# Kernel optimization log

Hardware: AMD Instinct MI355X
Metric: run time of the kernel (lower is better)

The kernel has to match this reference:

```python
import jax, jax.numpy as jnp
import numpy as np

N_NODES = 100000
N_EDGES = 1600000
IN_DIM = 256
OUT_DIM = 64
NEG_SLOPE = 0.01  # torch F.leaky_relu default


def setup_inputs() -> dict:
    key = jax.random.key(0)
    k1, k2, k3, k4, k5 = jax.random.split(key, 5)
    h = jax.random.normal(k1, (N_NODES, IN_DIM), dtype=jnp.float32)
    # Kaiming-ish small init for linear weights
    W = jax.random.normal(k2, (OUT_DIM, IN_DIM), dtype=jnp.float32) / np.sqrt(IN_DIM)
    A = jax.random.normal(k3, (1, 2 * OUT_DIM), dtype=jnp.float32) / np.sqrt(2 * OUT_DIM)
    src = jax.random.randint(k4, (N_EDGES,), 0, N_NODES, dtype=jnp.int32)
    dst = jax.random.randint(k5, (N_EDGES,), 0, N_NODES, dtype=jnp.int32)
    return {"h": h, "W": W, "A": A, "src": src, "dst": dst}


def reference(h, W, A, src, dst):
    n = h.shape[0]
    # fc (no bias): z = h @ W^T -> [N, out]
    z = h @ W.T
    # attn_fc on cat(z_src, z_dst): split A into src/dst halves to avoid concat
    a_src, a_dst = A[0, :OUT_DIM], A[0, OUT_DIM:]
    s_node = z @ a_src  # [N]
    d_node = z @ a_dst  # [N]
    e = s_node[src] + d_node[dst]  # [E] raw attention logits per edge
    e = jnp.where(e >= 0, e, NEG_SLOPE * e)  # leaky_relu
    # segment softmax over incoming edges of each dst node (numerically stable)
    e_max = jax.ops.segment_max(e, dst, num_segments=n)  # -inf for empty segments
    e_max = jnp.where(jnp.isfinite(e_max), e_max, 0.0)
    e_exp = jnp.exp(e - e_max[dst])
    denom = jax.ops.segment_sum(e_exp, dst, num_segments=n)
    alpha = e_exp / jnp.where(denom > 0, denom, 1.0)[dst]  # [E]
    # weighted scatter-sum of source features; nodes with no in-edges get 0
    out = jax.ops.segment_sum(alpha[:, None] * z[src], dst, num_segments=n)
    return out
```

## Files before the change

### kernel.cpp

```cpp
#include <hip/hip_runtime.h>

#define N_IN 256
#define N_OUT 64
#define NEG_SLOPE 0.01f
#define BSHIFT 9
#define BSIZE 512
#define MAXBUCK 256

typedef __attribute__((ext_vector_type(8))) short short8v;
typedef __attribute__((ext_vector_type(4))) float float4v;

__device__ inline short f32_to_bf16_rtne(float f) {
    unsigned u = __float_as_uint(f);
    unsigned r = (u + 0x7FFFu + ((u >> 16) & 1u)) >> 16;
    return (short)r;
}
__device__ inline float bf16_to_f32(short s) {
    return __uint_as_float(((unsigned)(unsigned short)s) << 16);
}

constexpr int GM = 64;
constexpr int KP = 264;

__global__ __launch_bounds__(256) void gemm_zsd_mfma(
    const float* __restrict__ h, const float* __restrict__ W,
    const float* __restrict__ A,
    unsigned short* __restrict__ zb, float* __restrict__ s_node, float* __restrict__ d_node,
    int n_nodes)
{
    __shared__ short hA[GM * KP];
    __shared__ short wB[N_OUT * KP];
    const int t = threadIdx.x;
    const int row0 = blockIdx.x * GM;

    for (int j = 0; j < 8; ++j) {
        const int f  = j * 256 + t;
        const int r  = f >> 5;
        const int c8 = f & 31;

        int grow = row0 + r;
        if (grow >= n_nodes) grow = n_nodes - 1;
        const float4* ph = reinterpret_cast<const float4*>(h + (size_t)grow * N_IN + c8 * 8);
        float4 h0 = ph[0], h1 = ph[1];
        short8v pkh;
        pkh[0] = f32_to_bf16_rtne(h0.x); pkh[1] = f32_to_bf16_rtne(h0.y);
        pkh[2] = f32_to_bf16_rtne(h0.z); pkh[3] = f32_to_bf16_rtne(h0.w);
        pkh[4] = f32_to_bf16_rtne(h1.x); pkh[5] = f32_to_bf16_rtne(h1.y);
        pkh[6] = f32_to_bf16_rtne(h1.z); pkh[7] = f32_to_bf16_rtne(h1.w);
        *reinterpret_cast<short8v*>(&hA[r * KP + c8 * 8]) = pkh;

        const float4* pw = reinterpret_cast<const float4*>(W + (size_t)r * N_IN + c8 * 8);
        float4 w0 = pw[0], w1 = pw[1];
        short8v pkw;
        pkw[0] = f32_to_bf16_rtne(w0.x); pkw[1] = f32_to_bf16_rtne(w0.y);
        pkw[2] = f32_to_bf16_rtne(w0.z); pkw[3] = f32_to_bf16_rtne(w0.w);
        pkw[4] = f32_to_bf16_rtne(w1.x); pkw[5] = f32_to_bf16_rtne(w1.y);
        pkw[6] = f32_to_bf16_rtne(w1.z); pkw[7] = f32_to_bf16_rtne(w1.w);
        *reinterpret_cast<short8v*>(&wB[r * KP + c8 * 8]) = pkw;
    }
    __syncthreads();

    const int w  = t >> 6;
    const int l  = t & 63;
    const int lr = l & 15;
    const int lk = l >> 4;

    float4v acc[4] = {{0.f,0.f,0.f,0.f},{0.f,0.f,0.f,0.f},
                      {0.f,0.f,0.f,0.f},{0.f,0.f,0.f,0.f}};

    for (int kk = 0; kk < 8; ++kk) {
        const int kbase = kk * 32 + lk * 8;
        const short8v a = *reinterpret_cast<const short8v*>(&hA[(w * 16 + lr) * KP + kbase]);
#pragma unroll
        for (int n = 0; n < 4; ++n) {
            const short8v b = *reinterpret_cast<const short8v*>(&wB[(n * 16 + lr) * KP + kbase]);
            acc[n] = __builtin_amdgcn_mfma_f32_16x16x32_bf16(a, b, acc[n], 0, 0, 0);
        }
    }

    float as[4], ad[4];
#pragma unroll
    for (int n = 0; n < 4; ++n) {
        as[n] = A[n * 16 + lr];
        ad[n] = A[N_OUT + n * 16 + lr];
    }

    float sv[4] = {0.f,0.f,0.f,0.f}, dv[4] = {0.f,0.f,0.f,0.f};
#pragma unroll
    for (int n = 0; n < 4; ++n) {
#pragma unroll
        for (int r = 0; r < 4; ++r) {
            const float v = acc[n][r];
            const int grow = row0 + w * 16 + lk * 4 + r;
            if (grow < n_nodes)
                zb[(size_t)grow * N_OUT + n * 16 + lr] = (unsigned short)f32_to_bf16_rtne(v);
            sv[r] = fmaf(v, as[n], sv[r]);
            dv[r] = fmaf(v, ad[n], dv[r]);
        }
    }
#pragma unroll
    for (int off = 1; off < 16; off <<= 1) {
#pragma unroll
        for (int r = 0; r < 4; ++r) {
            sv[r] += __shfl_xor(sv[r], off);
            dv[r] += __shfl_xor(dv[r], off);
        }
    }
    if (lr == 0) {
#pragma unroll
        for (int r = 0; r < 4; ++r) {
            const int grow = row0 + w * 16 + lk * 4 + r;
            if (grow < n_nodes) { s_node[grow] = sv[r]; d_node[grow] = dv[r]; }
        }
    }
}

__global__ __launch_bounds__(256) void hist_bucket(
    const int* __restrict__ dst, int* __restrict__ bcount, int n_edges)
{
    __shared__ int cnt[MAXBUCK];
    const int t = threadIdx.x;
    for (int i = t; i < MAXBUCK; i += 256) cnt[i] = 0;
    __syncthreads();
    int i = blockIdx.x * 256 + t;
    const int stride = gridDim.x * 256;
    for (; i < n_edges; i += stride)
        atomicAdd(&cnt[dst[i] >> BSHIFT], 1);
    __syncthreads();
    for (int j = t; j < MAXBUCK; j += 256)
        if (cnt[j]) atomicAdd(&bcount[j], cnt[j]);
}

__global__ __launch_bounds__(256) void scan_buckets(
    const int* __restrict__ bcount, int* __restrict__ bbase,
    int* __restrict__ bcursor, int nbuck, int n_edges)
{
    __shared__ int tmp[256];
    const int t = threadIdx.x;
    const int v = (t < nbuck) ? bcount[t] : 0;
    tmp[t] = v;
    __syncthreads();
    for (int off = 1; off < 256; off <<= 1) {
        int x = (t >= off) ? tmp[t - off] : 0;
        __syncthreads();
        tmp[t] += x;
        __syncthreads();
    }
    if (t < nbuck) {
        const int excl = tmp[t] - v;
        bbase[t] = excl;
        bcursor[t] = excl;
    }
    if (t == 0) bbase[nbuck] = n_edges;
}

__global__ __launch_bounds__(256) void bucket_scatter(
    const int* __restrict__ src, const int* __restrict__ dst,
    const float* __restrict__ s_node, const float* __restrict__ d_node,
    int* __restrict__ bcursor, int2* __restrict__ ebuf, int n_edges, int nbuck)
{
    __shared__ int cnt[MAXBUCK];
    __shared__ int wcur[MAXBUCK];
    const int t = threadIdx.x;
    const int chunk = (n_edges + gridDim.x - 1) / gridDim.x;
    const int lo = blockIdx.x * chunk;
    const int hi = min(lo + chunk, n_edges);

    for (int i = t; i < MAXBUCK; i += 256) cnt[i] = 0;
    __syncthreads();
    for (int i = lo + t; i < hi; i += 256)
        atomicAdd(&cnt[dst[i] >> BSHIFT], 1);
    __syncthreads();
    for (int i = t; i < nbuck; i += 256)
        wcur[i] = cnt[i] ? atomicAdd(&bcursor[i], cnt[i]) : 0;
    __syncthreads();
    for (int i = lo + t; i < hi; i += 256) {
        const int d = dst[i];
        const int s = src[i];
        float e = s_node[s] + d_node[d];
        e = (e >= 0.f) ? e : NEG_SLOPE * e;
        const float pe = __expf(e);
        const int b = d >> BSHIFT;
        const int pos = atomicAdd(&wcur[b], 1);
        ebuf[pos] = make_int2(((d & (BSIZE - 1)) << 23) | s, __float_as_int(pe));
    }
}

__global__ __launch_bounds__(1024) void bucket_bin(
    const int2* __restrict__ ebuf, const int* __restrict__ bbase,
    int2* __restrict__ ebuf2, int* __restrict__ segend, int n_nodes)
{
    __shared__ int dcnt[BSIZE];
    __shared__ int dscan[BSIZE];
    __shared__ int dcur[BSIZE];
    const int t = threadIdx.x;
    const int b = blockIdx.x;
    const int lo = bbase[b];
    const int hi = bbase[b + 1];

    if (t < BSIZE) dcnt[t] = 0;
    __syncthreads();
    for (int i = lo + t; i < hi; i += 1024)
        atomicAdd(&dcnt[((unsigned)ebuf[i].x) >> 23], 1);
    __syncthreads();
    const int v = (t < BSIZE) ? dcnt[t] : 0;
    if (t < BSIZE) dscan[t] = v;
    __syncthreads();
    for (int off = 1; off < BSIZE; off <<= 1) {
        int x = (t >= off && t < BSIZE) ? dscan[t - off] : 0;
        __syncthreads();
        if (t < BSIZE) dscan[t] += x;
        __syncthreads();
    }
    if (t < BSIZE) {
        const int d = b * BSIZE + t;
        if (d < n_nodes) segend[d] = lo + dscan[t];
        dcur[t] = lo + dscan[t] - v;
    }
    __syncthreads();
    for (int i = lo + t; i < hi; i += 1024) {
        const int2 e = ebuf[i];
        const unsigned x = (unsigned)e.x;
        const int pos = atomicAdd(&dcur[x >> 23], 1);
        ebuf2[pos] = make_int2((int)(x & 0x7FFFFFu), e.y);
    }
}

__global__ __launch_bounds__(256) void gather_accum(
    const int2* __restrict__ edges, const int* __restrict__ segend,
    const unsigned short* __restrict__ zb, float* __restrict__ out, int n_nodes)
{
    const int wave = (blockIdx.x * 256 + threadIdx.x) >> 6;
    const int lane = threadIdx.x & 63;
    if (wave >= n_nodes) return;
    const int sub = lane >> 3;
    const int l8  = lane & 7;
    const int end   = segend[wave];
    const int start = (wave == 0) ? 0 : segend[wave - 1];

    float acc[8] = {0.f,0.f,0.f,0.f,0.f,0.f,0.f,0.f};
    float denom = 0.f;
    int i = start + sub;
    for (; i + 8 < end; i += 16) {
        const int2 e0 = edges[i];
        const int2 e1 = edges[i + 8];
        const short8v z0 = *reinterpret_cast<const short8v*>(zb + (size_t)e0.x * N_OUT + l8 * 8);
        const short8v z1 = *reinterpret_cast<const short8v*>(zb + (size_t)e1.x * N_OUT + l8 * 8);
        const float p0 = __int_as_float(e0.y);
        const float p1 = __int_as_float(e1.y);
        denom += p0 + p1;
#pragma unroll
        for (int j = 0; j < 8; ++j) {
            acc[j] = fmaf(p0, bf16_to_f32(z0[j]), acc[j]);
            acc[j] = fmaf(p1, bf16_to_f32(z1[j]), acc[j]);
        }
    }
    for (; i < end; i += 8) {
        const int2 e0 = edges[i];
        const short8v z0 = *reinterpret_cast<const short8v*>(zb + (size_t)e0.x * N_OUT + l8 * 8);
        const float p0 = __int_as_float(e0.y);
        denom += p0;
#pragma unroll
        for (int j = 0; j < 8; ++j)
            acc[j] = fmaf(p0, bf16_to_f32(z0[j]), acc[j]);
    }
#pragma unroll
    for (int off = 8; off < 64; off <<= 1) {
#pragma unroll
        for (int j = 0; j < 8; ++j)
            acc[j] += __shfl_xor(acc[j], off);
        denom += __shfl_xor(denom, off);
    }
    if (sub == 0) {
        const float inv = (end > start) ? 1.f / denom : 0.f;
        float4 r0, r1;
        r0.x = acc[0] * inv; r0.y = acc[1] * inv; r0.z = acc[2] * inv; r0.w = acc[3] * inv;
        r1.x = acc[4] * inv; r1.y = acc[5] * inv; r1.z = acc[6] * inv; r1.w = acc[7] * inv;
        float4* po = reinterpret_cast<float4*>(out + (size_t)wave * N_OUT + l8 * 8);
        po[0] = r0; po[1] = r1;
    }
}

extern "C" void kernel_launch(void* const* d_in, const int* in_sizes, int n_in,
                              void* d_out, int out_size, void* d_ws, size_t ws_size,
                              hipStream_t stream) {
    const float* h = (const float*)d_in[0];
    const float* W = (const float*)d_in[1];
    const float* A = (const float*)d_in[2];
    const int* src = (const int*)d_in[3];
    const int* dst = (const int*)d_in[4];
    float* out = (float*)d_out;

    const int n_nodes = in_sizes[0] / N_IN;
    const int n_edges = in_sizes[3];
    const int nbuck = (n_nodes + BSIZE - 1) / BSIZE;

    char* ws = (char*)d_ws;
    unsigned short* zb = (unsigned short*)ws;  ws += (size_t)n_nodes * N_OUT * 2;
    float* s_node  = (float*)ws;  ws += (size_t)n_nodes * 4;
    float* d_node  = (float*)ws;  ws += (size_t)n_nodes * 4;
    int*   segend  = (int*)ws;    ws += (size_t)n_nodes * 4;
    int*   bcount  = (int*)ws;    ws += MAXBUCK * 4;
    int*   bbase   = (int*)ws;    ws += (MAXBUCK + 2) * 4;
    int*   bcursor = (int*)ws;    ws += MAXBUCK * 4;
    ws = (char*)(((uintptr_t)ws + 15) & ~(uintptr_t)15);
    int2*  ebuf    = (int2*)ws;   ws += (size_t)n_edges * 8;
    int2*  ebuf2   = (int2*)ws;

    hipMemsetAsync(bcount, 0, MAXBUCK * sizeof(int), stream);

    gemm_zsd_mfma<<<(n_nodes + GM - 1) / GM, 256, 0, stream>>>(h, W, A, zb, s_node, d_node, n_nodes);

    hist_bucket<<<256, 256, 0, stream>>>(dst, bcount, n_edges);

    scan_buckets<<<1, 256, 0, stream>>>(bcount, bbase, bcursor, nbuck, n_edges);

    bucket_scatter<<<256, 256, 0, stream>>>(src, dst, s_node, d_node, bcursor, ebuf, n_edges, nbuck);

    bucket_bin<<<nbuck, 1024, 0, stream>>>(ebuf, bbase, ebuf2, segend, n_nodes);

    gather_accum<<<(n_nodes * 64 + 255) / 256, 256, 0, stream>>>(ebuf2, segend, zb, out, n_nodes);
}
```

Before: 285.4 us.

## Fuse per-bucket binning with gather-accumulate, staging sorted edges in LDS

Merges the bucket_bin and gather_accum kernels into one bucket_gather kernel. Each block bins its bucket's edges by destination into shared memory, falling back to global memory when the bucket exceeds CAP, and then its 16 waves loop over the bucket's destination nodes to accumulate. Bucket size is halved to 256 nodes so a bucket's edges (about 4096 on average) fit in LDS, and the scan kernel is widened to handle up to 512 buckets. This removes the global write and re-read of the sorted edge list, the segend array, and one kernel launch. In exchange it runs far fewer, larger blocks for the gather phase, with imbalance between waves and heavy LDS use that may limit occupancy.

```diff
diff --git a/kernel.cpp b/kernel.cpp
--- a/kernel.cpp
+++ b/kernel.cpp
@@ -3,9 +3,10 @@
 #define N_IN 256
 #define N_OUT 64
 #define NEG_SLOPE 0.01f
-#define BSHIFT 9
-#define BSIZE 512
-#define MAXBUCK 256
+#define BSHIFT 8
+#define BSIZE 256
+#define MAXBUCK 512
+#define CAP 5120
 
 typedef __attribute__((ext_vector_type(8))) short short8v;
 typedef __attribute__((ext_vector_type(4))) float float4v;
@@ -131,16 +132,16 @@
         if (cnt[j]) atomicAdd(&bcount[j], cnt[j]);
 }
 
-__global__ __launch_bounds__(256) void scan_buckets(
+__global__ __launch_bounds__(1024) void scan_buckets(
     const int* __restrict__ bcount, int* __restrict__ bbase,
     int* __restrict__ bcursor, int nbuck, int n_edges)
 {
-    __shared__ int tmp[256];
+    __shared__ int tmp[1024];
     const int t = threadIdx.x;
     const int v = (t < nbuck) ? bcount[t] : 0;
     tmp[t] = v;
     __syncthreads();
-    for (int off = 1; off < 256; off <<= 1) {
+    for (int off = 1; off < 1024; off <<= 1) {
         int x = (t >= off) ? tmp[t - off] : 0;
         __syncthreads();
         tmp[t] += x;
@@ -186,10 +187,12 @@
     }
 }
 
-__global__ __launch_bounds__(1024) void bucket_bin(
+__global__ __launch_bounds__(1024) void bucket_gather(
     const int2* __restrict__ ebuf, const int* __restrict__ bbase,
-    int2* __restrict__ ebuf2, int* __restrict__ segend, int n_nodes)
-{
+    int2* __restrict__ ebuf2, const unsigned short* __restrict__ zb,
+    float* __restrict__ out, int n_nodes)
+{
+    __shared__ int2 sedge[CAP];
     __shared__ int dcnt[BSIZE];
     __shared__ int dscan[BSIZE];
     __shared__ int dcur[BSIZE];
@@ -197,87 +200,97 @@
     const int b = blockIdx.x;
     const int lo = bbase[b];
     const int hi = bbase[b + 1];
+    const int total = hi - lo;
 
     if (t < BSIZE) dcnt[t] = 0;
     __syncthreads();
     for (int i = lo + t; i < hi; i += 1024)
         atomicAdd(&dcnt[((unsigned)ebuf[i].x) >> 23], 1);
     __syncthreads();
-    const int v = (t < BSIZE) ? dcnt[t] : 0;
-    if (t < BSIZE) dscan[t] = v;
+    if (t < BSIZE) dscan[t] = dcnt[t];
     __syncthreads();
     for (int off = 1; off < BSIZE; off <<= 1) {
-        int x = (t >= off && t < BSIZE) ? dscan[t - off] : 0;
+        int x = (t < BSIZE && t >= off) ? dscan[t - off] : 0;
         __syncthreads();
         if (t < BSIZE) dscan[t] += x;
         __syncthreads();
     }
-    if (t < BSIZE) {
-        const int d = b * BSIZE + t;
-        if (d < n_nodes) segend[d] = lo + dscan[t];
-        dcur[t] = lo + dscan[t] - v;
-    }
-    __syncthreads();
-    for (int i = lo + t; i < hi; i += 1024) {
-        const int2 e = ebuf[i];
-        const unsigned x = (unsigned)e.x;
-        const int pos = atomicAdd(&dcur[x >> 23], 1);
-        ebuf2[pos] = make_int2((int)(x & 0x7FFFFFu), e.y);
-    }
-}
-
-__global__ __launch_bounds__(256) void gather_accum(
-    const int2* __restrict__ edges, const int* __restrict__ segend,
-    const unsigned short* __restrict__ zb, float* __restrict__ out, int n_nodes)
-{
-    const int wave = (blockIdx.x * 256 + threadIdx.x) >> 6;
-    const int lane = threadIdx.x & 63;
-    if (wave >= n_nodes) return;
-    const int sub = lane >> 3;
-    const int l8  = lane & 7;
-    const int end   = segend[wave];
-    const int start = (wave == 0) ? 0 : segend[wave - 1];
-
-    float acc[8] = {0.f,0.f,0.f,0.f,0.f,0.f,0.f,0.f};
-    float denom = 0.f;
-    int i = start + sub;
-    for (; i + 8 < end; i += 16) {
-        const int2 e0 = edges[i];
-        const int2 e1 = edges[i + 8];
-        const short8v z0 = *reinterpret_cast<const short8v*>(zb + (size_t)e0.x * N_OUT + l8 * 8);
-        const short8v z1 = *reinterpret_cast<const short8v*>(zb + (size_t)e1.x * N_OUT + l8 * 8);
-        const float p0 = __int_as_float(e0.y);
-        const float p1 = __int_as_float(e1.y);
-        denom += p0 + p1;
-#pragma unroll
-        for (int j = 0; j < 8; ++j) {
-            acc[j] = fmaf(p0, bf16_to_f32(z0[j]), acc[j]);
-            acc[j] = fmaf(p1, bf16_to_f32(z1[j]), acc[j]);
-        }
-    }
-    for (; i < end; i += 8) {
-        const int2 e0 = edges[i];
-        const short8v z0 = *reinterpret_cast<const short8v*>(zb + (size_t)e0.x * N_OUT + l8 * 8);
-        const float p0 = __int_as_float(e0.y);
-        denom += p0;
-#pragma unroll
-        for (int j = 0; j < 8; ++j)
-            acc[j] = fmaf(p0, bf16_to_f32(z0[j]), acc[j]);
-    }
-#pragma unroll
-    for (int off = 8; off < 64; off <<= 1) {
-#pragma unroll
-        for (int j = 0; j < 8; ++j)
-            acc[j] += __shfl_xor(acc[j], off);
-        denom += __shfl_xor(denom, off);
-    }
-    if (sub == 0) {
-        const float inv = (end > start) ? 1.f / denom : 0.f;
-        float4 r0, r1;
-        r0.x = acc[0] * inv; r0.y = acc[1] * inv; r0.z = acc[2] * inv; r0.w = acc[3] * inv;
-        r1.x = acc[4] * inv; r1.y = acc[5] * inv; r1.z = acc[6] * inv; r1.w = acc[7] * inv;
-        float4* po = reinterpret_cast<float4*>(out + (size_t)wave * N_OUT + l8 * 8);
-        po[0] = r0; po[1] = r1;
+    if (t < BSIZE) dcur[t] = dscan[t] - dcnt[t];
+    __syncthreads();
+
+    const int2* eptr;
+    if (total <= CAP) {
+        for (int i = lo + t; i < hi; i += 1024) {
+            const int2 e = ebuf[i];
+            const unsigned x = (unsigned)e.x;
+            const int pos = atomicAdd(&dcur[x >> 23], 1);
+            sedge[pos] = make_int2((int)(x & 0x7FFFFFu), e.y);
+        }
+        eptr = (const int2*)sedge;
+    } else {
+        for (int i = lo + t; i < hi; i += 1024) {
+            const int2 e = ebuf[i];
+            const unsigned x = (unsigned)e.x;
+            const int pos = atomicAdd(&dcur[x >> 23], 1);
+            ebuf2[lo + pos] = make_int2((int)(x & 0x7FFFFFu), e.y);
+        }
+        eptr = ebuf2 + lo;
+    }
+    __syncthreads();
+
+    const int wid  = t >> 6;
+    const int lane = t & 63;
+    const int sub  = lane >> 3;
+    const int l8   = lane & 7;
+
+    for (int d = wid; d < BSIZE; d += 16) {
+        const int gd = b * BSIZE + d;
+        if (gd >= n_nodes) break;
+        const int cnt = dcnt[d];
+        const int end = dscan[d];
+        const int start = end - cnt;
+
+        float acc[8] = {0.f,0.f,0.f,0.f,0.f,0.f,0.f,0.f};
+        float denom = 0.f;
+        int i = start + sub;
+        for (; i + 8 < end; i += 16) {
+            const int2 e0 = eptr[i];
+            const int2 e1 = eptr[i + 8];
+            const short8v z0 = *reinterpret_cast<const short8v*>(zb + (size_t)e0.x * N_OUT + l8 * 8);
+            const short8v z1 = *reinterpret_cast<const short8v*>(zb + (size_t)e1.x * N_OUT + l8 * 8);
+            const float p0 = __int_as_float(e0.y);
+            const float p1 = __int_as_float(e1.y);
+            denom += p0 + p1;
+#pragma unroll
+            for (int j = 0; j < 8; ++j) {
+                acc[j] = fmaf(p0, bf16_to_f32(z0[j]), acc[j]);
+                acc[j] = fmaf(p1, bf16_to_f32(z1[j]), acc[j]);
+            }
+        }
+        for (; i < end; i += 8) {
+            const int2 e0 = eptr[i];
+            const short8v z0 = *reinterpret_cast<const short8v*>(zb + (size_t)e0.x * N_OUT + l8 * 8);
+            const float p0 = __int_as_float(e0.y);
+            denom += p0;
+#pragma unroll
+            for (int j = 0; j < 8; ++j)
+                acc[j] = fmaf(p0, bf16_to_f32(z0[j]), acc[j]);
+        }
+#pragma unroll
+        for (int off = 8; off < 64; off <<= 1) {
+#pragma unroll
+            for (int j = 0; j < 8; ++j)
+                acc[j] += __shfl_xor(acc[j], off);
+            denom += __shfl_xor(denom, off);
+        }
+        if (sub == 0) {
+            const float inv = (cnt > 0) ? 1.f / denom : 0.f;
+            float4 r0, r1;
+            r0.x = acc[0] * inv; r0.y = acc[1] * inv; r0.z = acc[2] * inv; r0.w = acc[3] * inv;
+            r1.x = acc[4] * inv; r1.y = acc[5] * inv; r1.z = acc[6] * inv; r1.w = acc[7] * inv;
+            float4* po = reinterpret_cast<float4*>(out + (size_t)gd * N_OUT + l8 * 8);
+            po[0] = r0; po[1] = r1;
+        }
     }
 }
 
@@ -299,7 +312,6 @@
     unsigned short* zb = (unsigned short*)ws;  ws += (size_t)n_nodes * N_OUT * 2;
     float* s_node  = (float*)ws;  ws += (size_t)n_nodes * 4;
     float* d_node  = (float*)ws;  ws += (size_t)n_nodes * 4;
-    int*   segend  = (int*)ws;    ws += (size_t)n_nodes * 4;
     int*   bcount  = (int*)ws;    ws += MAXBUCK * 4;
     int*   bbase   = (int*)ws;    ws += (MAXBUCK + 2) * 4;
     int*   bcursor = (int*)ws;    ws += MAXBUCK * 4;
@@ -313,11 +325,9 @@
 
     hist_bucket<<<256, 256, 0, stream>>>(dst, bcount, n_edges);
 
-    scan_buckets<<<1, 256, 0, stream>>>(bcount, bbase, bcursor, nbuck, n_edges);
+    scan_buckets<<<1, 1024, 0, stream>>>(bcount, bbase, bcursor, nbuck, n_edges);
 
     bucket_scatter<<<256, 256, 0, stream>>>(src, dst, s_node, d_node, bcursor, ebuf, n_edges, nbuck);
 
-    bucket_bin<<<nbuck, 1024, 0, stream>>>(ebuf, bbase, ebuf2, segend, n_nodes);
-
-    gather_accum<<<(n_nodes * 64 + 255) / 256, 256, 0, stream>>>(ebuf2, segend, zb, out, n_nodes);
-}
+    bucket_gather<<<nbuck, 1024, 0, stream>>>(ebuf, bbase, ebuf2, zb, out, n_nodes);
+}
```

After: 288.2 us. No clear change (+1.0%).
